# Performance work log

Hardware: AMD Instinct MI355X
Metric: run time of the kernel (lower is better)

Reference implementation:

```python
import jax, jax.numpy as jnp
import numpy as np

N, D_IN, HID, NH = 16384, 2048, 2048, 16
HD = HID // NH  # head_size = 128


def setup_inputs() -> dict:
    key = jax.random.key(0)
    ks = jax.random.split(key, 8)
    s = 1.0 / np.sqrt(D_IN)
    return {
        "protein": jax.random.normal(ks[0], (N, D_IN), jnp.float32),
        "drug": jax.random.normal(ks[1], (N, D_IN), jnp.float32),
        "mask_prot": jnp.ones((N,), bool),
        "mask_drug": jnp.ones((N,), bool),
        "Wq_p": jax.random.uniform(ks[2], (D_IN, HID), jnp.float32, -s, s),
        "Wk_p": jax.random.uniform(ks[3], (D_IN, HID), jnp.float32, -s, s),
        "Wv_p": jax.random.uniform(ks[4], (D_IN, HID), jnp.float32, -s, s),
        "Wq_d": jax.random.uniform(ks[5], (D_IN, HID), jnp.float32, -s, s),
        "Wk_d": jax.random.uniform(ks[6], (D_IN, HID), jnp.float32, -s, s),
        "Wv_d": jax.random.uniform(ks[7], (D_IN, HID), jnp.float32, -s, s),
    }


def _heads(x):
    # [N, L, HID] -> [N, L, NH, HD]
    return x.reshape(x.shape[0], x.shape[1], NH, HD)


def _alpha_logits(logits, mask_row, mask_col, inf=1e6):
    # logits: [N, L1, L2, H]; masks: [N, L1], [N, L2] (broadcast over heads)
    mask_pair = mask_row[:, :, None, None] & mask_col[:, None, :, None]
    logits = jnp.where(mask_pair, logits, logits - inf)
    alpha = jax.nn.softmax(logits, axis=2)
    alpha = jnp.where(mask_row[:, :, None, None], alpha, jnp.zeros_like(alpha))
    return alpha


def reference(protein, drug, mask_prot, mask_drug, Wq_p, Wk_p, Wv_p, Wq_d, Wk_d, Wv_d):
    p = protein[:, None, :]  # [N, 1, D_IN]
    d = drug[:, None, :]
    # forward() overwrites the masks with all-ones of shape [N, L=1]
    m_p = jnp.ones(p.shape[:-1], bool)
    m_d = jnp.ones(d.shape[:-1], bool)

    qp = _heads(jnp.einsum('bld,dh->blh', p, Wq_p))  # [N,1,NH,HD]
    kp = _heads(jnp.einsum('bld,dh->blh', p, Wk_p))
    vp = _heads(jnp.einsum('bld,dh->blh', p, Wv_p))
    qd = _heads(jnp.einsum('bld,dh->blh', d, Wq_d))
    kd = _heads(jnp.einsum('bld,dh->blh', d, Wk_d))
    vd = _heads(jnp.einsum('bld,dh->blh', d, Wv_d))

    logits_pp = jnp.einsum('blhd,bkhd->blkh', qp, kp)
    logits_pd = jnp.einsum('blhd,bkhd->blkh', qp, kd)
    logits_dp = jnp.einsum('blhd,bkhd->blkh', qd, kp)
    logits_dd = jnp.einsum('blhd,bkhd->blkh', qd, kd)

    a_pp = _alpha_logits(logits_pp, m_p, m_p)
    a_pd = _alpha_logits(logits_pd, m_p, m_d)
    a_dp = _alpha_logits(logits_dp, m_d, m_p)
    a_dd = _alpha_logits(logits_dd, m_d, m_d)

    def agg(alpha, v):
        out = jnp.einsum('blkh,bkhd->blhd', alpha, v)
        return out.reshape(out.shape[0], out.shape[1], HID)

    prot_embedding = (agg(a_pp, vp) + agg(a_pd, vd)) / 2  # [N,1,HID]
    drug_embedding = (agg(a_dp, vp) + agg(a_dd, vd)) / 2

    # agg_mode == 'cls'
    prot_embed = prot_embedding[:, 0]
    drug_embed = drug_embedding[:, 0]
    return jnp.concatenate([prot_embed, drug_embed], axis=1)  # [N, 2*HID]
```

## Files before the change

kernel.cpp:

```cpp
#include <hip/hip_runtime.h>
#include <stdint.h>


typedef __attribute__((ext_vector_type(8))) short short8;
typedef __attribute__((ext_vector_type(4))) float float4v;
typedef __attribute__((ext_vector_type(2))) unsigned int uint2v;

typedef const __attribute__((address_space(1))) unsigned int* gp_t;
typedef __attribute__((address_space(3))) unsigned int* lp_t;

#define M_DIM 16384
#define N_DIM 2048
#define K_DIM 4096
#define OUT_LD 4096

static __device__ __forceinline__ unsigned int pack_bf16x2(float x, float y) {
  union { float f; unsigned int u; } a, b;
  a.f = x; b.f = y;
  unsigned int ua = a.u + 0x8000u;
  unsigned int ub = b.u + 0x8000u;
  return __builtin_amdgcn_perm(ub, ua, 0x07060302u);
}

static __device__ __forceinline__ unsigned short f2bf(float x) {
  union { float f; unsigned int u; } a; a.f = x;
  return (unsigned short)((a.u + 0x8000u) >> 16);
}

__global__ __launch_bounds__(256)
void prep_wt(const float* __restrict__ Wp, const float* __restrict__ Wd,
             unsigned short* __restrict__ Wt) {
  __shared__ float tile[32][33];
  const int k0 = blockIdx.x * 32;
  const int n0 = blockIdx.y * 32;
  const int tx = threadIdx.x;
  const int ty = threadIdx.y;
  const float* W = (k0 < 2048) ? Wp : Wd;
  const int kk0 = (k0 < 2048) ? k0 : k0 - 2048;
#pragma unroll
  for (int i = 0; i < 4; ++i) {
    int r = ty * 4 + i;
    tile[r][tx] = W[(size_t)(kk0 + r) * 2048 + n0 + tx];
  }
  __syncthreads();
#pragma unroll
  for (int i = 0; i < 4; ++i) {
    int r = ty * 4 + i;
    Wt[(size_t)(n0 + r) * (size_t)K_DIM + k0 + tx] = f2bf(tile[tx][r]);
  }
}

__global__ __launch_bounds__(256)
void cast_a(const float* __restrict__ P, const float* __restrict__ Dg,
            unsigned int* __restrict__ Abf) {
  int idx = blockIdx.x * 256 + threadIdx.x;
  int row = idx >> 10;
  int j = (idx & 1023) << 2;
  const float* src = (j < 2048) ? (P + (size_t)row * 2048 + j)
                                : (Dg + (size_t)row * 2048 + (j - 2048));
  float4v v = *(const float4v*)src;
  uint2v o;
  o.x = pack_bf16x2(v.x, v.y);
  o.y = pack_bf16x2(v.z, v.w);
  *(uint2v*)(Abf + (size_t)row * 2048 + (j >> 1)) = o;
}

template <bool ABF>
__global__ __launch_bounds__(256)
void gemm_k(const unsigned int* __restrict__ Abf,
            const float* __restrict__ Ap, const float* __restrict__ Ad,
            const unsigned short* __restrict__ Wt,
            float* __restrict__ out) {
  __shared__ unsigned short As[128 * 64];
  __shared__ unsigned short Bs[128 * 64];

  const int t = threadIdx.x;
  const int bx = blockIdx.x;
  const int tn = bx & 15, tm = bx >> 4;
  const int m0 = tm << 7, n0 = tn << 7;
  const int w = t >> 6, l = t & 63;
  const int wm = w & 1, wn = w >> 1;
  const int lr = l & 15, q = l >> 4;

  const int rB = t >> 3;
  const int kB = (t & 7) * 8;

  float4v acc[4][4];
#pragma unroll
  for (int i = 0; i < 4; ++i)
#pragma unroll
    for (int j = 0; j < 4; ++j)
      acc[i][j] = (float4v){0.f, 0.f, 0.f, 0.f};

  for (int k0 = 0; k0 < K_DIM; k0 += 64) {
#pragma unroll
    for (int i = 0; i < 4; ++i) {
      const unsigned short* g =
          Wt + (size_t)(n0 + i * 32 + rB) * (size_t)K_DIM + (k0 + kB);
      __builtin_amdgcn_global_load_lds((gp_t)(const void*)g,
                                       (lp_t)&Bs[i * 2048 + w * 512], 16, 0, 0);
    }
    if constexpr (ABF) {
#pragma unroll
      for (int i = 0; i < 4; ++i) {
        const unsigned int* g =
            Abf + ((size_t)(m0 + i * 32 + rB) * (size_t)K_DIM + (k0 + kB)) / 2;
        __builtin_amdgcn_global_load_lds((gp_t)(const void*)g,
                                         (lp_t)&As[i * 2048 + w * 512], 16, 0, 0);
      }
    } else {
      const float* base;
      int kk;
      if (k0 < 2048) { base = Ap; kk = k0; } else { base = Ad; kk = k0 - 2048; }
      const int rA = t >> 4;
      const int cA = (t & 15) * 4;
#pragma unroll
      for (int i = 0; i < 8; ++i) {
        int m = i * 16 + rA;
        float4v v = *(const float4v*)(base + (size_t)(m0 + m) * 2048 + kk + cA);
        uint2v o;
        o.x = pack_bf16x2(v.x, v.y);
        o.y = pack_bf16x2(v.z, v.w);
        *(uint2v*)&As[m * 64 + cA] = o;
      }
    }
    __syncthreads();

#pragma unroll
    for (int ks = 0; ks < 2; ++ks) {
      short8 af[4], bfr[4];
#pragma unroll
      for (int i = 0; i < 4; ++i) {
        af[i]  = *(const short8*)&As[(wm * 64 + i * 16 + lr) * 64 + ks * 32 + q * 8];
        bfr[i] = *(const short8*)&Bs[(wn * 64 + i * 16 + lr) * 64 + ks * 32 + q * 8];
      }
#pragma unroll
      for (int i = 0; i < 4; ++i)
#pragma unroll
        for (int j = 0; j < 4; ++j)
          acc[i][j] = __builtin_amdgcn_mfma_f32_16x16x32_bf16(af[i], bfr[j],
                                                              acc[i][j], 0, 0, 0);
    }
    __syncthreads();
  }

#pragma unroll
  for (int i = 0; i < 4; ++i) {
    const int r0 = m0 + wm * 64 + i * 16 + q * 4;
#pragma unroll
    for (int j = 0; j < 4; ++j) {
      const int c = n0 + wn * 64 + j * 16 + lr;
#pragma unroll
      for (int r = 0; r < 4; ++r) {
        float v = acc[i][j][r] * 0.5f;
        size_t o = (size_t)(r0 + r) * (size_t)OUT_LD + c;
        out[o] = v;
        out[o + 2048] = v;
      }
    }
  }
}

__global__ __launch_bounds__(256)
void gemm_fallback(const float* __restrict__ P, const float* __restrict__ Dg,
                   const float* __restrict__ Wp, const float* __restrict__ Wd,
                   float* __restrict__ out) {
  __shared__ float Asf[64][17];
  __shared__ float Bsf[16][65];
  const int bx = blockIdx.x;
  const int by = blockIdx.y;
  const int t = threadIdx.x;
  const int tc = t & 15, trw = t >> 4;
  const int m0 = by * 64, n0 = bx * 64;
  float accf[4][4] = {};
  for (int k0 = 0; k0 < 4096; k0 += 16) {
    const float* Asrc = (k0 < 2048) ? P : Dg;
    const float* Bsrc = (k0 < 2048) ? Wp : Wd;
    const int kk = k0 & 2047;
#pragma unroll
    for (int i = 0; i < 4; ++i) {
      int r = i * 16 + trw;
      Asf[r][tc] = Asrc[(size_t)(m0 + r) * 2048 + kk + tc];
    }
#pragma unroll
    for (int i = 0; i < 4; ++i) {
      int r = i * 4 + (t >> 6);
      int c = t & 63;
      Bsf[r][c] = Bsrc[(size_t)(kk + r) * 2048 + n0 + c];
    }
    __syncthreads();
#pragma unroll
    for (int k2 = 0; k2 < 16; ++k2) {
      float a[4], b[4];
#pragma unroll
      for (int i = 0; i < 4; ++i) a[i] = Asf[trw * 4 + i][k2];
#pragma unroll
      for (int j = 0; j < 4; ++j) b[j] = Bsf[k2][tc * 4 + j];
#pragma unroll
      for (int i = 0; i < 4; ++i)
#pragma unroll
        for (int j = 0; j < 4; ++j) accf[i][j] += a[i] * b[j];
    }
    __syncthreads();
  }
#pragma unroll
  for (int i = 0; i < 4; ++i)
#pragma unroll
    for (int j = 0; j < 4; ++j) {
      float v = accf[i][j] * 0.5f;
      size_t o = (size_t)(m0 + trw * 4 + i) * 4096 + n0 + tc * 4 + j;
      out[o] = v;
      out[o + 2048] = v;
    }
}

extern "C" void kernel_launch(void* const* d_in, const int* in_sizes, int n_in,
                              void* d_out, int out_size, void* d_ws, size_t ws_size,
                              hipStream_t stream) {
  const float* protein = (const float*)d_in[0];
  const float* drug    = (const float*)d_in[1];
  const float* Wv_p    = (const float*)d_in[6];
  const float* Wv_d    = (const float*)d_in[9];
  float* out = (float*)d_out;

  const size_t wt_bytes = (size_t)N_DIM * K_DIM * sizeof(unsigned short);
  const size_t a_bytes  = (size_t)M_DIM * K_DIM * sizeof(unsigned short);

  if (ws_size >= wt_bytes) {
    unsigned short* Wt = (unsigned short*)d_ws;
    prep_wt<<<dim3(128, 64), dim3(32, 8), 0, stream>>>(Wv_p, Wv_d, Wt);
    if (ws_size >= wt_bytes + a_bytes) {
      unsigned int* Abf = (unsigned int*)((char*)d_ws + wt_bytes);
      cast_a<<<65536, 256, 0, stream>>>(protein, drug, Abf);
      gemm_k<true><<<2048, 256, 0, stream>>>(Abf, nullptr, nullptr, Wt, out);
    } else {
      gemm_k<false><<<2048, 256, 0, stream>>>(nullptr, protein, drug, Wt, out);
    }
  } else {
    gemm_fallback<<<dim3(32, 256), 256, 0, stream>>>(protein, drug, Wv_p, Wv_d, out);
  }
}
```

Before: 827.4 us.

## Add 256x256 double-buffered bf16 GEMM with swizzled LDS and ping-pong scheduling

Replaces the 128x128 single-buffered bf16 GEMM with a 512-thread kernel that computes 256x256 tiles. It double-buffers A and B in LDS, XOR-swizzles the LDS columns to avoid bank conflicts, and interleaves global-to-LDS loads with four MFMA quadrant phases, using explicit waitcnt, barriers and setprio. The aim is to hide memory latency and raise data reuse per block. The cost is higher register and LDS use (128KB LDS per block with launch bounds 512,2) and a fragile hand-written pipeline.

```diff
diff --git a/kernel.cpp b/kernel.cpp
--- a/kernel.cpp
+++ b/kernel.cpp
@@ -65,21 +65,195 @@
   *(uint2v*)(Abf + (size_t)row * 2048 + (j >> 1)) = o;
 }
 
-template <bool ABF>
+
+#define VMW(N) asm volatile("s_waitcnt vmcnt(" #N ")" ::: "memory")
+#define LGW0() asm volatile("s_waitcnt lgkmcnt(0)" ::: "memory")
+#define BAR() __builtin_amdgcn_s_barrier()
+
+#define LOAD_A(Ac, QM)                                                      \
+  _Pragma("unroll") for (int i = 0; i < 4; ++i) {                           \
+    af[i][0] = *(const short8*)&(Ac)[aoff + ((QM)*4 + i) * 1024 + c0];      \
+    af[i][1] = *(const short8*)&(Ac)[aoff + ((QM)*4 + i) * 1024 + c1];      \
+  }
+
+#define LOAD_B(Bc, QN)                                                      \
+  _Pragma("unroll") for (int j = 0; j < 2; ++j) {                           \
+    bfr[j][0] = *(const short8*)&(Bc)[boff + ((QN)*2 + j) * 1024 + c0];     \
+    bfr[j][1] = *(const short8*)&(Bc)[boff + ((QN)*2 + j) * 1024 + c1];     \
+  }
+
+#define MFMA8(QM, QN)                                                       \
+  _Pragma("unroll") for (int i = 0; i < 4; ++i)                             \
+  _Pragma("unroll") for (int j = 0; j < 2; ++j) {                           \
+    acc[(QM)*4 + i][(QN)*2 + j] = __builtin_amdgcn_mfma_f32_16x16x32_bf16(  \
+        af[i][0], bfr[j][0], acc[(QM)*4 + i][(QN)*2 + j], 0, 0, 0);         \
+    acc[(QM)*4 + i][(QN)*2 + j] = __builtin_amdgcn_mfma_f32_16x16x32_bf16(  \
+        af[i][1], bfr[j][1], acc[(QM)*4 + i][(QN)*2 + j], 0, 0, 0);         \
+  }
+
+__global__ __launch_bounds__(512, 2)
+void gemm8(const unsigned short* __restrict__ Abf,
+           const unsigned short* __restrict__ Wt,
+           float* __restrict__ out) {
+  __shared__ unsigned short As[2][256 * 64];
+  __shared__ unsigned short Bs[2][256 * 64];
+
+  const int t = threadIdx.x;
+  const int w = t >> 6, l = t & 63;
+  const int wm = w >> 2, wn = w & 3;
+  const int lr = l & 15, q16 = l >> 4, xr = lr & 7;
+
+  const int bx = blockIdx.x;
+  const int tn = bx & 7, tm = bx >> 3;
+  const int m0 = tm << 8, n0 = tn << 8;
+
+  const int srow = t >> 3;
+  const int sk = (((t & 7) ^ (srow & 7)) << 3);
+  const int brr = srow & 31;
+  const int bsel = t >> 8;
+
+  auto stage_a = [&](int buf, int k0, int h) {
+#pragma unroll
+    for (int sub = 0; sub < 2; ++sub) {
+      const int row = m0 + sub * 128 + h * 64 + srow;
+      const unsigned short* g = Abf + (size_t)row * K_DIM + (k0 + sk);
+      const int ldsrow0 = sub * 128 + h * 64 + (w << 3);
+      __builtin_amdgcn_global_load_lds((gp_t)(const void*)g,
+                                       (lp_t)&As[buf][ldsrow0 * 64], 16, 0, 0);
+    }
+  };
+  auto stage_b = [&](int buf, int k0, int nh) {
+#pragma unroll
+    for (int sub = 0; sub < 2; ++sub) {
+      const int wnr = sub * 2 + bsel;
+      const int ncol = n0 + wnr * 64 + nh * 32 + brr;
+      const unsigned short* g = Wt + (size_t)ncol * K_DIM + (k0 + sk);
+      const int ldsrow0 = wnr * 64 + nh * 32 + ((w & 3) << 3);
+      __builtin_amdgcn_global_load_lds((gp_t)(const void*)g,
+                                       (lp_t)&Bs[buf][ldsrow0 * 64], 16, 0, 0);
+    }
+  };
+
+  float4v acc[8][4];
+#pragma unroll
+  for (int i = 0; i < 8; ++i)
+#pragma unroll
+    for (int j = 0; j < 4; ++j)
+      acc[i][j] = (float4v){0.f, 0.f, 0.f, 0.f};
+
+  const int aoff = (wm * 128 + lr) * 64;
+  const int boff = (wn * 64 + lr) * 64;
+  const int c0 = ((q16) ^ xr) << 3;
+  const int c1 = ((4 + q16) ^ xr) << 3;
+
+  stage_a(0, 0, 0);
+  stage_b(0, 0, 0);
+  stage_b(0, 0, 1);
+  stage_a(0, 0, 1);
+  stage_a(1, 64, 0);
+  stage_b(1, 64, 0);
+  VMW(8);
+  BAR();
+
+  for (int tt = 0; tt < 62; ++tt) {
+    const int buf = tt & 1;
+    unsigned short* Ac = &As[buf][0];
+    unsigned short* Bc = &Bs[buf][0];
+    const int k1 = tt * 64 + 64;
+    const int k2 = tt * 64 + 128;
+    short8 af[4][2];
+    short8 bfr[2][2];
+
+    LOAD_A(Ac, 0)
+    LOAD_B(Bc, 0)
+    stage_b(buf ^ 1, k1, 1);
+    VMW(8); BAR(); LGW0();
+    __builtin_amdgcn_s_setprio(1);
+    MFMA8(0, 0)
+    __builtin_amdgcn_s_setprio(0);
+    BAR();
+
+    LOAD_B(Bc, 1)
+    stage_a(buf ^ 1, k1, 1);
+    VMW(8); BAR(); LGW0();
+    __builtin_amdgcn_s_setprio(1);
+    MFMA8(0, 1)
+    __builtin_amdgcn_s_setprio(0);
+    BAR();
+
+    LOAD_A(Ac, 1)
+    LOAD_B(Bc, 0)
+    stage_a(buf, k2, 0);
+    VMW(8); BAR(); LGW0();
+    __builtin_amdgcn_s_setprio(1);
+    MFMA8(1, 0)
+    __builtin_amdgcn_s_setprio(0);
+    BAR();
+
+    LOAD_B(Bc, 1)
+    stage_b(buf, k2, 0);
+    VMW(8); BAR(); LGW0();
+    __builtin_amdgcn_s_setprio(1);
+    MFMA8(1, 1)
+    __builtin_amdgcn_s_setprio(0);
+    BAR();
+  }
+
+  stage_b(1, 4032, 1);
+  stage_a(1, 4032, 1);
+  VMW(0);
+  BAR();
+#pragma unroll
+  for (int e = 0; e < 2; ++e) {
+    unsigned short* Ac = &As[e][0];
+    unsigned short* Bc = &Bs[e][0];
+    short8 af[4][2];
+    short8 bfr[2][2];
+    __builtin_amdgcn_s_setprio(1);
+    LOAD_A(Ac, 0)
+    LOAD_B(Bc, 0)
+    MFMA8(0, 0)
+    LOAD_B(Bc, 1)
+    MFMA8(0, 1)
+    LOAD_A(Ac, 1)
+    LOAD_B(Bc, 0)
+    MFMA8(1, 0)
+    LOAD_B(Bc, 1)
+    MFMA8(1, 1)
+    __builtin_amdgcn_s_setprio(0);
+  }
+
+  const int rbase = m0 + wm * 128 + q16 * 4;
+  const int cbase = n0 + wn * 64 + lr;
+#pragma unroll
+  for (int f = 0; f < 8; ++f)
+#pragma unroll
+    for (int j = 0; j < 4; ++j) {
+      const int row = rbase + f * 16;
+      const int col = cbase + j * 16;
+#pragma unroll
+      for (int r = 0; r < 4; ++r) {
+        float v = acc[f][j][r] * 0.5f;
+        size_t o = (size_t)(row + r) * (size_t)OUT_LD + col;
+        out[o] = v;
+        out[o + N_DIM] = v;
+      }
+    }
+}
+
 __global__ __launch_bounds__(256)
-void gemm_k(const unsigned int* __restrict__ Abf,
-            const float* __restrict__ Ap, const float* __restrict__ Ad,
+void gemm_k(const float* __restrict__ Ap, const float* __restrict__ Ad,
             const unsigned short* __restrict__ Wt,
             float* __restrict__ out) {
   __shared__ unsigned short As[128 * 64];
-  __shared__ unsigned short Bs[128 * 64];
+  __shared__ unsigned short Bsm[128 * 64];
 
   const int t = threadIdx.x;
   const int bx = blockIdx.x;
   const int tn = bx & 15, tm = bx >> 4;
   const int m0 = tm << 7, n0 = tn << 7;
   const int w = t >> 6, l = t & 63;
-  const int wm = w & 1, wn = w >> 1;
+  const int wmm = w & 1, wnn = w >> 1;
   const int lr = l & 15, q = l >> 4;
 
   const int rB = t >> 3;
@@ -98,17 +272,9 @@
       const unsigned short* g =
           Wt + (size_t)(n0 + i * 32 + rB) * (size_t)K_DIM + (k0 + kB);
       __builtin_amdgcn_global_load_lds((gp_t)(const void*)g,
-                                       (lp_t)&Bs[i * 2048 + w * 512], 16, 0, 0);
-    }
-    if constexpr (ABF) {
-#pragma unroll
-      for (int i = 0; i < 4; ++i) {
-        const unsigned int* g =
-            Abf + ((size_t)(m0 + i * 32 + rB) * (size_t)K_DIM + (k0 + kB)) / 2;
-        __builtin_amdgcn_global_load_lds((gp_t)(const void*)g,
-                                         (lp_t)&As[i * 2048 + w * 512], 16, 0, 0);
-      }
-    } else {
+                                       (lp_t)&Bsm[i * 2048 + w * 512], 16, 0, 0);
+    }
+    {
       const float* base;
       int kk;
       if (k0 < 2048) { base = Ap; kk = k0; } else { base = Ad; kk = k0 - 2048; }
@@ -128,17 +294,17 @@
 
 #pragma unroll
     for (int ks = 0; ks < 2; ++ks) {
-      short8 af[4], bfr[4];
+      short8 a2[4], b2[4];
 #pragma unroll
       for (int i = 0; i < 4; ++i) {
-        af[i]  = *(const short8*)&As[(wm * 64 + i * 16 + lr) * 64 + ks * 32 + q * 8];
-        bfr[i] = *(const short8*)&Bs[(wn * 64 + i * 16 + lr) * 64 + ks * 32 + q * 8];
+        a2[i] = *(const short8*)&As[(wmm * 64 + i * 16 + lr) * 64 + ks * 32 + q * 8];
+        b2[i] = *(const short8*)&Bsm[(wnn * 64 + i * 16 + lr) * 64 + ks * 32 + q * 8];
       }
 #pragma unroll
       for (int i = 0; i < 4; ++i)
 #pragma unroll
         for (int j = 0; j < 4; ++j)
-          acc[i][j] = __builtin_amdgcn_mfma_f32_16x16x32_bf16(af[i], bfr[j],
+          acc[i][j] = __builtin_amdgcn_mfma_f32_16x16x32_bf16(a2[i], b2[j],
                                                               acc[i][j], 0, 0, 0);
     }
     __syncthreads();
@@ -146,10 +312,10 @@
 
 #pragma unroll
   for (int i = 0; i < 4; ++i) {
-    const int r0 = m0 + wm * 64 + i * 16 + q * 4;
+    const int r0 = m0 + wmm * 64 + i * 16 + q * 4;
 #pragma unroll
     for (int j = 0; j < 4; ++j) {
-      const int c = n0 + wn * 64 + j * 16 + lr;
+      const int c = n0 + wnn * 64 + j * 16 + lr;
 #pragma unroll
       for (int r = 0; r < 4; ++r) {
         float v = acc[i][j][r] * 0.5f;
@@ -232,9 +398,9 @@
     if (ws_size >= wt_bytes + a_bytes) {
       unsigned int* Abf = (unsigned int*)((char*)d_ws + wt_bytes);
       cast_a<<<65536, 256, 0, stream>>>(protein, drug, Abf);
-      gemm_k<true><<<2048, 256, 0, stream>>>(Abf, nullptr, nullptr, Wt, out);
+      gemm8<<<512, 512, 0, stream>>>((const unsigned short*)Abf, Wt, out);
     } else {
-      gemm_k<false><<<2048, 256, 0, stream>>>(nullptr, protein, drug, Wt, out);
+      gemm_k<<<2048, 256, 0, stream>>>(protein, drug, Wt, out);
     }
   } else {
     gemm_fallback<<<dim3(32, 256), 256, 0, stream>>>(protein, drug, Wv_p, Wv_d, out);
```

Result: faster. 807.5 us (-2.4%).
